# Kernel tuning notes

Measured on AMD Instinct MI355X. Metric: run time of the kernel, lower is better.

Reference implementation:

```python
import jax, jax.numpy as jnp
import numpy as np

B, IN, HID, OUT, E = 8192, 1024, 4096, 1024, 8
EPS = 1e-5  # torch LayerNorm default


def _layernorm(x, gamma, beta):
    # normalize over last axis; gamma/beta broadcast as [E, dim] against [B, E, dim]
    mu = jnp.mean(x, axis=-1, keepdims=True)
    var = jnp.var(x, axis=-1, keepdims=True)
    return (x - mu) * jax.lax.rsqrt(var + EPS) * gamma + beta


def setup_inputs() -> dict:
    key = jax.random.key(0)
    ks = jax.random.split(key, 8)
    x = jax.random.normal(ks[0], (B, IN), dtype=jnp.float32)
    weights = jax.random.uniform(ks[1], (B, E), dtype=jnp.float32)
    s1 = 1.0 / np.sqrt(IN)
    s2 = 1.0 / np.sqrt(HID)
    W1 = jax.random.uniform(ks[2], (E, IN, HID), minval=-s1, maxval=s1, dtype=jnp.float32)
    b1 = jax.random.uniform(ks[3], (E, HID), minval=-s1, maxval=s1, dtype=jnp.float32)
    W2 = jax.random.uniform(ks[4], (E, HID, OUT), minval=-s2, maxval=s2, dtype=jnp.float32)
    b2 = jax.random.uniform(ks[5], (E, OUT), minval=-s2, maxval=s2, dtype=jnp.float32)
    g1 = jnp.ones((E, HID), dtype=jnp.float32)
    be1 = jnp.zeros((E, HID), dtype=jnp.float32)
    g2 = jnp.ones((E, OUT), dtype=jnp.float32)
    be2 = jnp.zeros((E, OUT), dtype=jnp.float32)
    return {"x": x, "weights": weights, "W1": W1, "b1": b1, "g1": g1, "be1": be1,
            "W2": W2, "b2": b2, "g2": g2, "be2": be2}


def reference(x, weights, W1, b1, g1, be1, W2, b2, g2, be2):
    # Each expert MLP([1024,4096,1024]): Linear -> LN -> GELU -> Linear -> LN -> GELU
    # (MLP appends LayerNorm + activation after EVERY Linear, including the last).
    # Dropout p=0 / eval mode -> identity. All experts run on every token.
    h = jnp.einsum('bi,eih->beh', x, W1) + b1          # [B, E, HID]
    h = jax.nn.gelu(_layernorm(h, g1, be1), approximate=False)
    y = jnp.einsum('beh,eho->beo', h, W2) + b2         # [B, E, OUT]
    y = jax.nn.gelu(_layernorm(y, g2, be2), approximate=False)
    # weighted combine: einsum('bij,bi->bj')
    return jnp.einsum('beo,be->bo', y, weights)        # [B, OUT]
```

## Files before the change

kernel.cpp:

```cpp
#include <hip/hip_runtime.h>
#include <cstdint>
#include <cstddef>

typedef unsigned short u16;
typedef float f32x4 __attribute__((ext_vector_type(4)));
typedef __bf16 bf16x8 __attribute__((ext_vector_type(8)));

#define B_DIM   8192
#define IN_DIM  1024
#define HID_DIM 4096
#define OUT_DIM 1024
#define NEXP    8

__device__ __forceinline__ u16 f2b(float f) {
    uint32_t u = __builtin_bit_cast(uint32_t, f);
    u += 0x7fffu + ((u >> 16) & 1u);
    return (u16)(u >> 16);
}
__device__ __forceinline__ float b2f(u16 b) {
    uint32_t u = ((uint32_t)b) << 16;
    return __builtin_bit_cast(float, u);
}
__device__ __forceinline__ float gelu_fast(float x) {
    float y = x * (0.7978845608f + 0.03567740814f * x * x);
    float a = fminf(y * 2.8853900818f, 80.0f);
    float e = __builtin_amdgcn_exp2f(a);
    return x * e * __builtin_amdgcn_rcpf(e + 1.0f);
}
__device__ __forceinline__ void async_cp16(const void* g, void* l) {
    __builtin_amdgcn_global_load_lds(
        (const __attribute__((address_space(1))) void*)g,
        (__attribute__((address_space(3))) void*)l,
        16, 0, 0);
}

__global__ __launch_bounds__(256)
void cvt_bf16(const float* __restrict__ in, u16* __restrict__ out, int n4) {
    int i = blockIdx.x * 256 + threadIdx.x;
    if (i >= n4) return;
    float4 v = *(const float4*)&in[(size_t)i * 4];
    uint2 o;
    o.x = (uint32_t)f2b(v.x) | ((uint32_t)f2b(v.y) << 16);
    o.y = (uint32_t)f2b(v.z) | ((uint32_t)f2b(v.w) << 16);
    *(uint2*)&out[(size_t)i * 4] = o;
}

__global__ __launch_bounds__(256)
void transpose_cvt2(const float* __restrict__ W1e, u16* __restrict__ w1t,
                    const float* __restrict__ W2e, u16* __restrict__ w2t) {
    __shared__ float tile[32][33];
    const float* W; u16* Wt; int K, N, n0, k0;
    if (blockIdx.z == 0) {
        W = W1e; Wt = w1t; K = IN_DIM; N = HID_DIM;
        n0 = blockIdx.x * 32; k0 = blockIdx.y * 32;
    } else {
        W = W2e; Wt = w2t; K = HID_DIM; N = OUT_DIM;
        n0 = blockIdx.y * 32; k0 = blockIdx.x * 32;
    }
    const int tx = threadIdx.x & 31, ty = threadIdx.x >> 5;
#pragma unroll
    for (int i = 0; i < 4; ++i) {
        int k = k0 + ty + i * 8;
        tile[ty + i * 8][tx] = W[(size_t)k * N + n0 + tx];
    }
    __syncthreads();
#pragma unroll
    for (int i = 0; i < 4; ++i) {
        int n = n0 + ty + i * 8;
        Wt[(size_t)n * K + k0 + tx] = f2b(tile[tx][ty + i * 8]);
    }
}

template<int F32OUT>
__global__ __launch_bounds__(512, 2)
void gemm256_pipe(const u16* __restrict__ A, const u16* __restrict__ Bt,
                  const float* __restrict__ bias, void* __restrict__ Cv,
                  int M, int N, int lda, int ldb, int Ksl) {
    __shared__ __attribute__((aligned(16))) u16 sA[4][256 * 32];
    __shared__ __attribute__((aligned(16))) u16 sB[4][256 * 32];

    const int tid  = threadIdx.x;
    const int wid  = tid >> 6;
    const int lane = tid & 63;
    const int quad = lane >> 4;
    const int lr   = lane & 15;
    const int wm   = wid >> 2;
    const int wn   = wid & 3;
    const int z    = blockIdx.z;

    const int NX = gridDim.x, NY = gridDim.y;
    const int bid = blockIdx.y * NX + blockIdx.x;
    const int xcd = bid & 7;
    const int j   = bid >> 3;
    const int yl  = j / NX;
    const int bx  = j - yl * NX;
    const int by  = xcd * (NY >> 3) + yl;

    const int m0 = by * 256;
    const int n0 = bx * 256;

    const int sr  = lane >> 2;
    const int scl = ((lane & 3) ^ ((lane >> 3) & 3)) * 8;
    const int qsw = (lr >> 1) & 3;

    const u16* Ag0 = A  + ((size_t)z * Ksl) + ((size_t)m0 + wid * 16 + sr) * (size_t)lda + scl;
    const u16* Ag1 = Ag0 + (size_t)128 * lda;
    const u16* Bg0 = Bt + ((size_t)z * Ksl) + ((size_t)n0 + wid * 16 + sr) * (size_t)ldb + scl;
    const u16* Bg1 = Bg0 + (size_t)128 * ldb;

    const int rdA = (wm * 128 + lr) * 32 + ((quad ^ qsw) * 8);
    const int rdB = (wn * 64  + lr) * 32 + ((quad ^ qsw) * 8);

    const int NT = Ksl >> 5;

#define STAGE(tt) do {                                                        \
        const int sl_ = (tt) & 3;                                             \
        const size_t ko_ = (size_t)(tt) * 32;                                 \
        async_cp16(Ag0 + ko_, &sA[sl_][wid * 512]);                           \
        async_cp16(Ag1 + ko_, &sA[sl_][4096 + wid * 512]);                    \
        async_cp16(Bg0 + ko_, &sB[sl_][wid * 512]);                           \
        async_cp16(Bg1 + ko_, &sB[sl_][4096 + wid * 512]);                    \
    } while (0)

#define READF(afd, bfd, tt) do {                                              \
        const u16* sa_ = &sA[(tt) & 3][0];                                    \
        const u16* sb_ = &sB[(tt) & 3][0];                                    \
        _Pragma("unroll")                                                     \
        for (int mi = 0; mi < 8; ++mi)                                        \
            afd[mi] = *(const bf16x8*)&sa_[rdA + mi * 512];                   \
        _Pragma("unroll")                                                     \
        for (int ni = 0; ni < 4; ++ni)                                        \
            bfd[ni] = *(const bf16x8*)&sb_[rdB + ni * 512];                   \
    } while (0)

#define CLUSTER(afc, bfc) do {                                                \
        __builtin_amdgcn_s_setprio(1);                                        \
        _Pragma("unroll")                                                     \
        for (int mi = 0; mi < 8; ++mi)                                        \
            _Pragma("unroll")                                                 \
            for (int ni = 0; ni < 4; ++ni)                                    \
                acc[mi][ni] = __builtin_amdgcn_mfma_f32_16x16x32_bf16(        \
                    afc[mi], bfc[ni], acc[mi][ni], 0, 0, 0);                  \
        __builtin_amdgcn_s_setprio(0);                                        \
    } while (0)

#define BODY(tt, afc, bfc, afn, bfn) do {                                     \
        const int pre_ = (tt) + 3;                                            \
        if (pre_ < NT) STAGE(pre_);                                           \
        READF(afn, bfn, (tt) + 1);                                            \
        CLUSTER(afc, bfc);                                                    \
        if (pre_ < NT) asm volatile("s_waitcnt vmcnt(4)" ::: "memory");       \
        else           asm volatile("s_waitcnt vmcnt(0)" ::: "memory");       \
        asm volatile("s_barrier" ::: "memory");                               \
    } while (0)

    STAGE(0); STAGE(1); STAGE(2);
    asm volatile("s_waitcnt vmcnt(4)" ::: "memory");
    asm volatile("s_barrier" ::: "memory");

    bf16x8 afA[8], bfA[4], afB[8], bfB[4];
    READF(afA, bfA, 0);

    f32x4 acc[8][4] = {};

#pragma unroll 1
    for (int t = 0; t < NT - 2; t += 2) {
        BODY(t,     afA, bfA, afB, bfB);
        BODY(t + 1, afB, bfB, afA, bfA);
    }
    BODY(NT - 2, afA, bfA, afB, bfB);
    CLUSTER(afB, bfB);

#undef BODY
#undef CLUSTER
#undef READF
#undef STAGE

    if constexpr (F32OUT) {
        float* C = (float*)Cv + (size_t)z * ((size_t)M * N);
#pragma unroll
        for (int mi = 0; mi < 8; ++mi) {
            const int mr = m0 + wm * 128 + mi * 16 + quad * 4;
#pragma unroll
            for (int r = 0; r < 4; ++r) {
                float* Crow = C + (size_t)(mr + r) * N + n0 + wn * 64 + lr;
#pragma unroll
                for (int ni = 0; ni < 4; ++ni)
                    Crow[ni * 16] = acc[mi][ni][r];
            }
        }
    } else {
        u16* C = (u16*)Cv;
        float bvv[4];
#pragma unroll
        for (int ni = 0; ni < 4; ++ni)
            bvv[ni] = bias[n0 + wn * 64 + ni * 16 + lr];
#pragma unroll
        for (int mi = 0; mi < 8; ++mi) {
            const int mr = m0 + wm * 128 + mi * 16 + quad * 4;
#pragma unroll
            for (int r = 0; r < 4; ++r) {
                u16* Crow = C + (size_t)(mr + r) * N + n0 + wn * 64 + lr;
#pragma unroll
                for (int ni = 0; ni < 4; ++ni)
                    Crow[ni * 16] = f2b(acc[mi][ni][r] + bvv[ni]);
            }
        }
    }
}

__global__ __launch_bounds__(256)
void gemm_bt_bias(const u16* __restrict__ A, const u16* __restrict__ Bt,
                  const float* __restrict__ bias, u16* __restrict__ C,
                  int M, int N, int K) {
    __shared__ __attribute__((aligned(16))) u16 sA[2][128 * 32];
    __shared__ __attribute__((aligned(16))) u16 sB[2][128 * 32];

    const int tid  = threadIdx.x;
    const int wid  = tid >> 6;
    const int lane = tid & 63;
    const int quad = lane >> 4;
    const int lr   = lane & 15;
    const int wm   = wid & 1;
    const int wn   = wid >> 1;

    const int NX = gridDim.x, NY = gridDim.y;
    const int bid = blockIdx.y * NX + blockIdx.x;
    const int xcd = bid & 7;
    const int j   = bid >> 3;
    const int yl  = j / NX;
    const int bx  = j - yl * NX;
    const int by  = xcd * (NY >> 3) + yl;

    const int m0 = by * 128;
    const int n0 = bx * 128;

    const int sr  = lane >> 2;
    const int scl = ((lane & 3) ^ ((lane >> 3) & 3)) * 8;
    const int qsw = (lr >> 1) & 3;

    const u16* Ag = A + (size_t)m0 * K;
    const u16* Bg = Bt + (size_t)n0 * K;

    f32x4 acc[4][4] = {};

    for (int k0 = 0; k0 < K; k0 += 64) {
#pragma unroll
        for (int s = 0; s < 2; ++s) {
#pragma unroll
            for (int i = 0; i < 2; ++i) {
                const int rb = wid * 32 + i * 16;
                async_cp16(Ag + (size_t)(rb + sr) * K + k0 + s * 32 + scl,
                           &sA[s][rb * 32]);
                async_cp16(Bg + (size_t)(rb + sr) * K + k0 + s * 32 + scl,
                           &sB[s][rb * 32]);
            }
        }
        __syncthreads();

#pragma unroll
        for (int s = 0; s < 2; ++s) {
            bf16x8 af[4], bfr[4];
#pragma unroll
            for (int mi = 0; mi < 4; ++mi)
                af[mi] = *(const bf16x8*)
                    &sA[s][(wm * 64 + mi * 16 + lr) * 32 + ((quad ^ qsw) * 8)];
#pragma unroll
            for (int ni = 0; ni < 4; ++ni)
                bfr[ni] = *(const bf16x8*)
                    &sB[s][(wn * 64 + ni * 16 + lr) * 32 + ((quad ^ qsw) * 8)];

#pragma unroll
            for (int mi = 0; mi < 4; ++mi)
#pragma unroll
                for (int ni = 0; ni < 4; ++ni)
                    acc[mi][ni] = __builtin_amdgcn_mfma_f32_16x16x32_bf16(
                        af[mi], bfr[ni], acc[mi][ni], 0, 0, 0);
        }

        __syncthreads();
    }

    float bvv[4];
#pragma unroll
    for (int ni = 0; ni < 4; ++ni)
        bvv[ni] = bias[n0 + wn * 64 + ni * 16 + lr];

#pragma unroll
    for (int mi = 0; mi < 4; ++mi) {
        const int mr = m0 + wm * 64 + mi * 16 + quad * 4;
#pragma unroll
        for (int r = 0; r < 4; ++r) {
            u16* Crow = C + (size_t)(mr + r) * N + n0 + wn * 64 + lr;
#pragma unroll
            for (int ni = 0; ni < 4; ++ni)
                Crow[ni * 16] = f2b(acc[mi][ni][r] + bvv[ni]);
        }
    }
}

__global__ __launch_bounds__(256)
void ln_gelu_hid(u16* __restrict__ h, const float* __restrict__ g,
                 const float* __restrict__ be) {
    __shared__ float red[8];
    const int row = blockIdx.x;
    u16* hp = h + (size_t)row * HID_DIM;
    const int t = threadIdx.x;

    uint4 v0 = *(const uint4*)&hp[t * 8];
    uint4 v1 = *(const uint4*)&hp[(t + 256) * 8];

    float vals[16];
    {
        const uint32_t w0[4] = {v0.x, v0.y, v0.z, v0.w};
        const uint32_t w1[4] = {v1.x, v1.y, v1.z, v1.w};
#pragma unroll
        for (int q = 0; q < 4; ++q) {
            vals[q * 2]     = b2f((u16)(w0[q] & 0xffffu));
            vals[q * 2 + 1] = b2f((u16)(w0[q] >> 16));
            vals[8 + q * 2]     = b2f((u16)(w1[q] & 0xffffu));
            vals[8 + q * 2 + 1] = b2f((u16)(w1[q] >> 16));
        }
    }
    float s = 0.f, ss = 0.f;
#pragma unroll
    for (int i = 0; i < 16; ++i) { s += vals[i]; ss += vals[i] * vals[i]; }

    float4 gv[4], bv[4];
    gv[0] = *(const float4*)&g[t * 8];
    gv[1] = *(const float4*)&g[t * 8 + 4];
    gv[2] = *(const float4*)&g[(t + 256) * 8];
    gv[3] = *(const float4*)&g[(t + 256) * 8 + 4];
    bv[0] = *(const float4*)&be[t * 8];
    bv[1] = *(const float4*)&be[t * 8 + 4];
    bv[2] = *(const float4*)&be[(t + 256) * 8];
    bv[3] = *(const float4*)&be[(t + 256) * 8 + 4];

#pragma unroll
    for (int off = 32; off > 0; off >>= 1) {
        s += __shfl_down(s, off, 64);
        ss += __shfl_down(ss, off, 64);
    }
    if ((t & 63) == 0) { red[(t >> 6) * 2] = s; red[(t >> 6) * 2 + 1] = ss; }
    __syncthreads();
    s  = red[0] + red[2] + red[4] + red[6];
    ss = red[1] + red[3] + red[5] + red[7];
    const float mean = s * (1.f / HID_DIM);
    const float rstd = rsqrtf(ss * (1.f / HID_DIM) - mean * mean + 1e-5f);

    const float* gf = (const float*)gv;
    const float* bf = (const float*)bv;
#pragma unroll
    for (int j = 0; j < 2; ++j) {
        uint4 o;
        uint32_t* ow = (uint32_t*)&o;
#pragma unroll
        for (int q = 0; q < 4; ++q) {
            const int k = j * 8 + q * 2;
            float u0 = gelu_fast((vals[k]     - mean) * rstd * gf[k]     + bf[k]);
            float u1 = gelu_fast((vals[k + 1] - mean) * rstd * gf[k + 1] + bf[k + 1]);
            ow[q] = (uint32_t)f2b(u0) | ((uint32_t)f2b(u1) << 16);
        }
        *(uint4*)&hp[(t + j * 256) * 8] = o;
    }
}

__global__ __launch_bounds__(256)
void ln_gelu_combine(const u16* __restrict__ y, const float* __restrict__ g,
                     const float* __restrict__ be, const float* __restrict__ wts,
                     float* __restrict__ out, int e, int first) {
    __shared__ float red[8];
    const int row = blockIdx.x;
    const u16* yp = y + (size_t)row * OUT_DIM;
    const int t = threadIdx.x;

    uint2 v = *(const uint2*)&yp[t * 4];
    float f0 = b2f((u16)(v.x & 0xffffu)), f1 = b2f((u16)(v.x >> 16));
    float f2 = b2f((u16)(v.y & 0xffffu)), f3 = b2f((u16)(v.y >> 16));
    float s = f0 + f1 + f2 + f3;
    float ss = f0 * f0 + f1 * f1 + f2 * f2 + f3 * f3;

    const int n = t * 4;
    float4 gv = *(const float4*)&g[n];
    float4 bvv = *(const float4*)&be[n];

#pragma unroll
    for (int off = 32; off > 0; off >>= 1) {
        s += __shfl_down(s, off, 64);
        ss += __shfl_down(ss, off, 64);
    }
    if ((t & 63) == 0) { red[(t >> 6) * 2] = s; red[(t >> 6) * 2 + 1] = ss; }
    __syncthreads();
    s  = red[0] + red[2] + red[4] + red[6];
    ss = red[1] + red[3] + red[5] + red[7];
    const float mean = s * (1.f / OUT_DIM);
    const float rstd = rsqrtf(ss * (1.f / OUT_DIM) - mean * mean + 1e-5f);

    const float w = wts[(size_t)row * NEXP + e];
    float4 o;
    if (first) { o.x = o.y = o.z = o.w = 0.f; }
    else       { o = *(const float4*)&out[(size_t)row * OUT_DIM + n]; }
    o.x += w * gelu_fast((f0 - mean) * rstd * gv.x + bvv.x);
    o.y += w * gelu_fast((f1 - mean) * rstd * gv.y + bvv.y);
    o.z += w * gelu_fast((f2 - mean) * rstd * gv.z + bvv.z);
    o.w += w * gelu_fast((f3 - mean) * rstd * gv.w + bvv.w);
    *(float4*)&out[(size_t)row * OUT_DIM + n] = o;
}

__global__ __launch_bounds__(256)
void ln_gelu_combine_f32(const float* __restrict__ P, const float* __restrict__ g,
                         const float* __restrict__ be, const float* __restrict__ bs,
                         const float* __restrict__ wts, float* __restrict__ out,
                         int e, int first) {
    __shared__ float red[8];
    const int row = blockIdx.x;
    const int t = threadIdx.x;
    const int n = t * 4;

    const float* p0 = P + (size_t)row * OUT_DIM + n;
    const float* p1 = p0 + (size_t)B_DIM * OUT_DIM;
    float4 a  = *(const float4*)p0;
    float4 b  = *(const float4*)p1;
    float4 c  = *(const float4*)&bs[n];
    float f0 = a.x + b.x + c.x, f1 = a.y + b.y + c.y;
    float f2 = a.z + b.z + c.z, f3 = a.w + b.w + c.w;
    float s = f0 + f1 + f2 + f3;
    float ss = f0 * f0 + f1 * f1 + f2 * f2 + f3 * f3;

    float4 gv = *(const float4*)&g[n];
    float4 bvv = *(const float4*)&be[n];

#pragma unroll
    for (int off = 32; off > 0; off >>= 1) {
        s += __shfl_down(s, off, 64);
        ss += __shfl_down(ss, off, 64);
    }
    if ((t & 63) == 0) { red[(t >> 6) * 2] = s; red[(t >> 6) * 2 + 1] = ss; }
    __syncthreads();
    s  = red[0] + red[2] + red[4] + red[6];
    ss = red[1] + red[3] + red[5] + red[7];
    const float mean = s * (1.f / OUT_DIM);
    const float rstd = rsqrtf(ss * (1.f / OUT_DIM) - mean * mean + 1e-5f);

    const float w = wts[(size_t)row * NEXP + e];
    float4 o;
    if (first) { o.x = o.y = o.z = o.w = 0.f; }
    else       { o = *(const float4*)&out[(size_t)row * OUT_DIM + n]; }
    o.x += w * gelu_fast((f0 - mean) * rstd * gv.x + bvv.x);
    o.y += w * gelu_fast((f1 - mean) * rstd * gv.y + bvv.y);
    o.z += w * gelu_fast((f2 - mean) * rstd * gv.z + bvv.z);
    o.w += w * gelu_fast((f3 - mean) * rstd * gv.w + bvv.w);
    *(float4*)&out[(size_t)row * OUT_DIM + n] = o;
}

extern "C" void kernel_launch(void* const* d_in, const int* in_sizes, int n_in,
                              void* d_out, int out_size, void* d_ws, size_t ws_size,
                              hipStream_t stream) {
    (void)in_sizes; (void)n_in; (void)out_size;
    const float* x   = (const float*)d_in[0];
    const float* wts = (const float*)d_in[1];
    const float* W1  = (const float*)d_in[2];
    const float* b1  = (const float*)d_in[3];
    const float* g1  = (const float*)d_in[4];
    const float* be1 = (const float*)d_in[5];
    const float* W2  = (const float*)d_in[6];
    const float* b2  = (const float*)d_in[7];
    const float* g2  = (const float*)d_in[8];
    const float* be2 = (const float*)d_in[9];
    float* out = (float*)d_out;

    char* p = (char*)d_ws;
    u16* xb  = (u16*)p; p += (size_t)B_DIM * IN_DIM * 2;
    u16* w1t = (u16*)p; p += (size_t)HID_DIM * IN_DIM * 2;
    u16* w2t = (u16*)p; p += (size_t)OUT_DIM * HID_DIM * 2;
    u16* h   = (u16*)p; p += (size_t)B_DIM * HID_DIM * 2;
    float* P = (float*)p;
    u16*  y  = (u16*)p;

    const size_t need = (size_t)B_DIM * IN_DIM * 2 + (size_t)HID_DIM * IN_DIM * 2 +
                        (size_t)OUT_DIM * HID_DIM * 2 + (size_t)B_DIM * HID_DIM * 2 +
                        (size_t)2 * B_DIM * OUT_DIM * 4;
    const int splitk = (ws_size >= need) ? 1 : 0;

    cvt_bf16<<<(B_DIM * IN_DIM / 4 + 255) / 256, 256, 0, stream>>>(x, xb, B_DIM * IN_DIM / 4);

    for (int e = 0; e < NEXP; ++e) {
        transpose_cvt2<<<dim3(HID_DIM / 32, IN_DIM / 32, 2), 256, 0, stream>>>(
            W1 + (size_t)e * IN_DIM * HID_DIM, w1t,
            W2 + (size_t)e * HID_DIM * OUT_DIM, w2t);
        gemm256_pipe<0><<<dim3(HID_DIM / 256, B_DIM / 256, 1), 512, 0, stream>>>(
            xb, w1t, b1 + (size_t)e * HID_DIM, h, B_DIM, HID_DIM, IN_DIM, IN_DIM, IN_DIM);
        ln_gelu_hid<<<B_DIM, 256, 0, stream>>>(h, g1 + (size_t)e * HID_DIM,
                                               be1 + (size_t)e * HID_DIM);
        if (splitk) {
            gemm256_pipe<1><<<dim3(OUT_DIM / 256, B_DIM / 256, 2), 512, 0, stream>>>(
                h, w2t, nullptr, P, B_DIM, OUT_DIM, HID_DIM, HID_DIM, HID_DIM / 2);
            ln_gelu_combine_f32<<<B_DIM, 256, 0, stream>>>(
                P, g2 + (size_t)e * OUT_DIM, be2 + (size_t)e * OUT_DIM,
                b2 + (size_t)e * OUT_DIM, wts, out, e, e == 0 ? 1 : 0);
        } else {
            gemm_bt_bias<<<dim3(OUT_DIM / 128, B_DIM / 128), 256, 0, stream>>>(
                h, w2t, b2 + (size_t)e * OUT_DIM, y, B_DIM, OUT_DIM, HID_DIM);
            ln_gelu_combine<<<B_DIM, 256, 0, stream>>>(y, g2 + (size_t)e * OUT_DIM,
                                                       be2 + (size_t)e * OUT_DIM, wts, out,
                                                       e, e == 0 ? 1 : 0);
        }
    }
}
```

Before: 1.936 ms.

## Restructure bf16 GEMM main loop into eight-phase interleaved load/MFMA schedule

Replaces the 4-slot, 32-wide K pipeline with a 64-wide K double-buffered scheme in which each iteration is split into four phases. Each phase reads a small slice of A/B fragments from LDS, issues part of the next tile's global-to-LDS copies, then runs a barrier-synchronised cluster of 16 MFMAs. The aim is finer interleaving of memory traffic and compute and lower register pressure, since only 4+4 fragments are live instead of two sets of 8+4. In exchange it adds many more barriers per K step, which may serialise the waves.

```diff
diff --git a/kernel.cpp b/kernel.cpp
--- a/kernel.cpp
+++ b/kernel.cpp
@@ -73,11 +73,11 @@
 
 template<int F32OUT>
 __global__ __launch_bounds__(512, 2)
-void gemm256_pipe(const u16* __restrict__ A, const u16* __restrict__ Bt,
-                  const float* __restrict__ bias, void* __restrict__ Cv,
-                  int M, int N, int lda, int ldb, int Ksl) {
-    __shared__ __attribute__((aligned(16))) u16 sA[4][256 * 32];
-    __shared__ __attribute__((aligned(16))) u16 sB[4][256 * 32];
+void gemm256_8ph(const u16* __restrict__ A, const u16* __restrict__ Bt,
+                 const float* __restrict__ bias, void* __restrict__ Cv,
+                 int M, int N, int lda, int ldb, int Ksl) {
+    __shared__ __attribute__((aligned(16))) u16 sA[32768];
+    __shared__ __attribute__((aligned(16))) u16 sB[32768];
 
     const int tid  = threadIdx.x;
     const int wid  = tid >> 6;
@@ -95,86 +95,104 @@
     const int yl  = j / NX;
     const int bx  = j - yl * NX;
     const int by  = xcd * (NY >> 3) + yl;
-
     const int m0 = by * 256;
     const int n0 = bx * 256;
 
-    const int sr  = lane >> 2;
-    const int scl = ((lane & 3) ^ ((lane >> 3) & 3)) * 8;
-    const int qsw = (lr >> 1) & 3;
-
-    const u16* Ag0 = A  + ((size_t)z * Ksl) + ((size_t)m0 + wid * 16 + sr) * (size_t)lda + scl;
-    const u16* Ag1 = Ag0 + (size_t)128 * lda;
-    const u16* Bg0 = Bt + ((size_t)z * Ksl) + ((size_t)n0 + wid * 16 + sr) * (size_t)ldb + scl;
-    const u16* Bg1 = Bg0 + (size_t)128 * ldb;
+    const int qsw   = (lr >> 1) & 3;
+    const int row_s = tid >> 2;
+    const int lc    = ((tid & 3) ^ ((tid >> 3) & 3)) * 8;
+
+    const u16* Ast = A  + (size_t)z * Ksl + (size_t)(m0 + row_s) * lda + lc;
+    const u16* Bst = Bt + (size_t)z * Ksl + (size_t)(n0 + row_s) * ldb + lc;
 
     const int rdA = (wm * 128 + lr) * 32 + ((quad ^ qsw) * 8);
     const int rdB = (wn * 64  + lr) * 32 + ((quad ^ qsw) * 8);
-
-    const int NT = Ksl >> 5;
-
-#define STAGE(tt) do {                                                        \
-        const int sl_ = (tt) & 3;                                             \
-        const size_t ko_ = (size_t)(tt) * 32;                                 \
-        async_cp16(Ag0 + ko_, &sA[sl_][wid * 512]);                           \
-        async_cp16(Ag1 + ko_, &sA[sl_][4096 + wid * 512]);                    \
-        async_cp16(Bg0 + ko_, &sB[sl_][wid * 512]);                           \
-        async_cp16(Bg1 + ko_, &sB[sl_][4096 + wid * 512]);                    \
+    const int d0  = tid * 8;
+
+    const int NT = Ksl >> 6;
+
+    f32x4 acc[8][4] = {};
+    bf16x8 av[4], bv[4];
+
+#define STG_A(hb, ko) do {                                                     \
+        async_cp16(Ast + (ko),                      &sA[(hb) + d0]);           \
+        async_cp16(Ast + (ko) + (size_t)128 * lda,  &sA[(hb) + d0 + 4096]);    \
     } while (0)
-
-#define READF(afd, bfd, tt) do {                                              \
-        const u16* sa_ = &sA[(tt) & 3][0];                                    \
-        const u16* sb_ = &sB[(tt) & 3][0];                                    \
-        _Pragma("unroll")                                                     \
-        for (int mi = 0; mi < 8; ++mi)                                        \
-            afd[mi] = *(const bf16x8*)&sa_[rdA + mi * 512];                   \
-        _Pragma("unroll")                                                     \
-        for (int ni = 0; ni < 4; ++ni)                                        \
-            bfd[ni] = *(const bf16x8*)&sb_[rdB + ni * 512];                   \
+#define STG_B(hb, ko) do {                                                     \
+        async_cp16(Bst + (ko),                      &sB[(hb) + d0]);           \
+        async_cp16(Bst + (ko) + (size_t)128 * ldb,  &sB[(hb) + d0 + 4096]);    \
     } while (0)
-
-#define CLUSTER(afc, bfc) do {                                                \
-        __builtin_amdgcn_s_setprio(1);                                        \
-        _Pragma("unroll")                                                     \
-        for (int mi = 0; mi < 8; ++mi)                                        \
-            _Pragma("unroll")                                                 \
-            for (int ni = 0; ni < 4; ++ni)                                    \
-                acc[mi][ni] = __builtin_amdgcn_mfma_f32_16x16x32_bf16(        \
-                    afc[mi], bfc[ni], acc[mi][ni], 0, 0, 0);                  \
-        __builtin_amdgcn_s_setprio(0);                                        \
+#define RD_A4(hb, MO) do { _Pragma("unroll")                                   \
+        for (int mi_ = 0; mi_ < 4; ++mi_)                                      \
+            av[mi_] = *(const bf16x8*)&sA[(hb) + rdA + ((MO) + mi_) * 512];    \
     } while (0)
-
-#define BODY(tt, afc, bfc, afn, bfn) do {                                     \
-        const int pre_ = (tt) + 3;                                            \
-        if (pre_ < NT) STAGE(pre_);                                           \
-        READF(afn, bfn, (tt) + 1);                                            \
-        CLUSTER(afc, bfc);                                                    \
-        if (pre_ < NT) asm volatile("s_waitcnt vmcnt(4)" ::: "memory");       \
-        else           asm volatile("s_waitcnt vmcnt(0)" ::: "memory");       \
-        asm volatile("s_barrier" ::: "memory");                               \
+#define RD_B4(hb) do { _Pragma("unroll")                                       \
+        for (int ni_ = 0; ni_ < 4; ++ni_)                                      \
+            bv[ni_] = *(const bf16x8*)&sB[(hb) + rdB + ni_ * 512];             \
     } while (0)
-
-    STAGE(0); STAGE(1); STAGE(2);
-    asm volatile("s_waitcnt vmcnt(4)" ::: "memory");
-    asm volatile("s_barrier" ::: "memory");
-
-    bf16x8 afA[8], bfA[4], afB[8], bfB[4];
-    READF(afA, bfA, 0);
-
-    f32x4 acc[8][4] = {};
+#define SYNC_MFMA16(MO) do {                                                   \
+        __builtin_amdgcn_s_barrier();                                          \
+        asm volatile("s_waitcnt lgkmcnt(0)");                                  \
+        __builtin_amdgcn_sched_barrier(0);                                     \
+        __builtin_amdgcn_s_setprio(1);                                         \
+        _Pragma("unroll")                                                      \
+        for (int mi_ = 0; mi_ < 4; ++mi_)                                      \
+            _Pragma("unroll")                                                  \
+            for (int ni_ = 0; ni_ < 4; ++ni_)                                  \
+                acc[(MO) + mi_][ni_] = __builtin_amdgcn_mfma_f32_16x16x32_bf16(\
+                    av[mi_], bv[ni_], acc[(MO) + mi_][ni_], 0, 0, 0);          \
+        __builtin_amdgcn_s_setprio(0);                                         \
+    } while (0)
+
+    STG_A(0, 0);      STG_B(0, 0);
+    STG_A(8192, 32);  STG_B(8192, 32);
+    asm volatile("s_waitcnt vmcnt(4)");
+    __builtin_amdgcn_s_barrier();
 
 #pragma unroll 1
-    for (int t = 0; t < NT - 2; t += 2) {
-        BODY(t,     afA, bfA, afB, bfB);
-        BODY(t + 1, afB, bfB, afA, bfA);
-    }
-    BODY(NT - 2, afA, bfA, afB, bfB);
-    CLUSTER(afB, bfB);
-
-#undef BODY
-#undef CLUSTER
-#undef READF
-#undef STAGE
+    for (int t = 0; t < NT - 1; ++t) {
+        const int cb = (t & 1) << 14;
+        const int nb = cb ^ 16384;
+        const size_t kt = (size_t)(t + 1) * 64;
+        RD_A4(cb, 0); RD_B4(cb);
+        STG_A(nb, kt);
+        SYNC_MFMA16(0);
+        __builtin_amdgcn_s_barrier();
+        RD_A4(cb, 4);
+        STG_B(nb, kt);
+        SYNC_MFMA16(4);
+        asm volatile("s_waitcnt vmcnt(4)");
+        __builtin_amdgcn_s_barrier();
+        RD_A4(cb + 8192, 0); RD_B4(cb + 8192);
+        STG_A(nb + 8192, kt + 32);
+        SYNC_MFMA16(0);
+        __builtin_amdgcn_s_barrier();
+        RD_A4(cb + 8192, 4);
+        STG_B(nb + 8192, kt + 32);
+        SYNC_MFMA16(4);
+        asm volatile("s_waitcnt vmcnt(4)");
+        __builtin_amdgcn_s_barrier();
+    }
+    {
+        const int cb = ((NT - 1) & 1) << 14;
+        RD_A4(cb, 0); RD_B4(cb);
+        SYNC_MFMA16(0);
+        __builtin_amdgcn_s_barrier();
+        RD_A4(cb, 4);
+        SYNC_MFMA16(4);
+        asm volatile("s_waitcnt vmcnt(0)");
+        __builtin_amdgcn_s_barrier();
+        RD_A4(cb + 8192, 0); RD_B4(cb + 8192);
+        SYNC_MFMA16(0);
+        __builtin_amdgcn_s_barrier();
+        RD_A4(cb + 8192, 4);
+        SYNC_MFMA16(4);
+    }
+#undef SYNC_MFMA16
+#undef RD_B4
+#undef RD_A4
+#undef STG_B
+#undef STG_A
 
     if constexpr (F32OUT) {
         float* C = (float*)Cv + (size_t)z * ((size_t)M * N);
@@ -488,12 +506,12 @@
         transpose_cvt2<<<dim3(HID_DIM / 32, IN_DIM / 32, 2), 256, 0, stream>>>(
             W1 + (size_t)e * IN_DIM * HID_DIM, w1t,
             W2 + (size_t)e * HID_DIM * OUT_DIM, w2t);
-        gemm256_pipe<0><<<dim3(HID_DIM / 256, B_DIM / 256, 1), 512, 0, stream>>>(
+        gemm256_8ph<0><<<dim3(HID_DIM / 256, B_DIM / 256, 1), 512, 0, stream>>>(
             xb, w1t, b1 + (size_t)e * HID_DIM, h, B_DIM, HID_DIM, IN_DIM, IN_DIM, IN_DIM);
         ln_gelu_hid<<<B_DIM, 256, 0, stream>>>(h, g1 + (size_t)e * HID_DIM,
                                                be1 + (size_t)e * HID_DIM);
         if (splitk) {
-            gemm256_pipe<1><<<dim3(OUT_DIM / 256, B_DIM / 256, 2), 512, 0, stream>>>(
+            gemm256_8ph<1><<<dim3(OUT_DIM / 256, B_DIM / 256, 2), 512, 0, stream>>>(
                 h, w2t, nullptr, P, B_DIM, OUT_DIM, HID_DIM, HID_DIM, HID_DIM / 2);
             ln_gelu_combine_f32<<<B_DIM, 256, 0, stream>>>(
                 P, g2 + (size_t)e * OUT_DIM, be2 + (size_t)e * OUT_DIM,
```

Result: faster. 1.862 ms (-3.9%).
